# Optimization experiments

Measured on AMD Instinct MI355X. Metric: run time of the kernel, lower is better.

The kernel has to match this reference:

```python
import jax, jax.numpy as jnp
import numpy as np


def _scan(x):
    # x: [B, C, D0, D1, D2] -> [B, 4, C, L] with L = D0*D1*D2
    B, C = x.shape[0], x.shape[1]
    x0 = x.reshape(B, C, -1)                          # row-major flatten of (D0,D1,D2)
    x1 = jnp.swapaxes(x, -2, -1).reshape(B, C, -1)    # swap last two spatial axes then flatten
    x2 = jnp.flip(x0, axis=-1)
    x3 = jnp.flip(x1, axis=-1)
    return jnp.stack([x0, x1, x2, x3], axis=1)        # [B, 4, C, L]


def setup_inputs() -> dict:
    key = jax.random.key(0)
    x = jax.random.normal(key, (2, 96, 32, 32, 32), dtype=jnp.float32)
    return {"x": x}


def reference(x) -> jnp.ndarray:
    # x: [B, C, I, J, K]
    xs_i = _scan(x)                                   # scan over (i, j, k)
    xs_j = _scan(jnp.transpose(x, (0, 1, 3, 4, 2)))   # b c i j k -> b c j k i
    xs_k = _scan(jnp.transpose(x, (0, 1, 4, 2, 3)))   # b c i j k -> b c k i j
    return jnp.concatenate([xs_i, xs_j, xs_k], axis=1)  # [B, 12, C, I*J*K]
```

## Files before the change

### kernel.cpp

```cpp
#include <hip/hip_runtime.h>

#define L 32768
#define NC 96
#define LDS_FLOATS (32 * 1057)
#define LDS_BYTES  (LDS_FLOATS * 4)

typedef float f4 __attribute__((ext_vector_type(4)));


__global__ __launch_bounds__(1024) void cross_scan3d(const float* __restrict__ in,
                                                     float* __restrict__ out) {
    extern __shared__ float lds[];

    const int bc  = blockIdx.x;
    const int b   = bc / NC;
    const int c   = bc % NC;
    const int tid = threadIdx.x;

    const f4* src4 = (const f4*)(in + (size_t)bc * L);
    #define OPTR(s) ((f4*)(out + ((size_t)((b)*12 + (s)) * NC + (c)) * L))
    #define NT(p, v) __builtin_nontemporal_store((v), (p))
    #define A(i, j, k) ((i) * 1057 + (j) * 33 + (k))

    f4* o0 = OPTR(0);  f4* o0f = OPTR(2);
    f4* o1 = OPTR(1);  f4* o1f = OPTR(3);
    f4* o2 = OPTR(4);  f4* o2f = OPTR(6);
    f4* o3 = OPTR(5);  f4* o3f = OPTR(7);
    f4* o4 = OPTR(8);  f4* o4f = OPTR(10);
    f4* o5 = OPTR(9);  f4* o5f = OPTR(11);

    #pragma unroll
    for (int it = 0; it < 8; ++it) {
        int t = it * 1024 + tid;
        f4 v = src4[t];
        int i = t >> 8, j = (t >> 3) & 31, k4 = t & 7;
        float* d = &lds[A(i, j, k4 * 4)];
        d[0] = v.x; d[1] = v.y; d[2] = v.z; d[3] = v.w;
        NT(o0 + t, v);
        f4 vr = { v.w, v.z, v.y, v.x };
        NT(o0f + (8191 - t), vr);
    }
    __syncthreads();

    #pragma unroll
    for (int it = 0; it < 8; ++it) {
        int t = it * 1024 + tid;
        int i = t >> 8, k = (t >> 3) & 31, j4 = t & 7;
        f4 v;
        v.x = lds[A(i, j4 * 4 + 0, k)];
        v.y = lds[A(i, j4 * 4 + 1, k)];
        v.z = lds[A(i, j4 * 4 + 2, k)];
        v.w = lds[A(i, j4 * 4 + 3, k)];
        NT(o1 + t, v);
        f4 vr = { v.w, v.z, v.y, v.x };
        NT(o1f + (8191 - t), vr);
    }

    #pragma unroll
    for (int it = 0; it < 8; ++it) {
        int t = it * 1024 + tid;
        int j = t >> 8, i = (t >> 3) & 31, k4 = t & 7;
        f4 v;
        v.x = lds[A(i, j, k4 * 4 + 0)];
        v.y = lds[A(i, j, k4 * 4 + 1)];
        v.z = lds[A(i, j, k4 * 4 + 2)];
        v.w = lds[A(i, j, k4 * 4 + 3)];
        NT(o3 + t, v);
        f4 vr = { v.w, v.z, v.y, v.x };
        NT(o3f + (8191 - t), vr);
    }

    #pragma unroll
    for (int it = 0; it < 8; ++it) {
        int t = it * 1024 + tid;
        int j = t >> 8, k = (t >> 3) & 31, i4 = t & 7;
        f4 v;
        v.x = lds[A(i4 * 4 + 0, j, k)];
        v.y = lds[A(i4 * 4 + 1, j, k)];
        v.z = lds[A(i4 * 4 + 2, j, k)];
        v.w = lds[A(i4 * 4 + 3, j, k)];
        NT(o2 + t, v);
        f4 vr = { v.w, v.z, v.y, v.x };
        NT(o2f + (8191 - t), vr);
    }

    #pragma unroll
    for (int it = 0; it < 8; ++it) {
        int t = it * 1024 + tid;
        int k = t >> 8, i = (t >> 3) & 31, j4 = t & 7;
        f4 v;
        v.x = lds[A(i, j4 * 4 + 0, k)];
        v.y = lds[A(i, j4 * 4 + 1, k)];
        v.z = lds[A(i, j4 * 4 + 2, k)];
        v.w = lds[A(i, j4 * 4 + 3, k)];
        NT(o4 + t, v);
        f4 vr = { v.w, v.z, v.y, v.x };
        NT(o4f + (8191 - t), vr);
    }

    #pragma unroll
    for (int it = 0; it < 8; ++it) {
        int t = it * 1024 + tid;
        int k = t >> 8, j = (t >> 3) & 31, i4 = t & 7;
        f4 v;
        v.x = lds[A(i4 * 4 + 0, j, k)];
        v.y = lds[A(i4 * 4 + 1, j, k)];
        v.z = lds[A(i4 * 4 + 2, j, k)];
        v.w = lds[A(i4 * 4 + 3, j, k)];
        NT(o5 + t, v);
        f4 vr = { v.w, v.z, v.y, v.x };
        NT(o5f + (8191 - t), vr);
    }

    #undef OPTR
    #undef NT
    #undef A
}

extern "C" void kernel_launch(void* const* d_in, const int* in_sizes, int n_in,
                              void* d_out, int out_size, void* d_ws, size_t ws_size,
                              hipStream_t stream) {
    const float* in = (const float*)d_in[0];
    float* out = (float*)d_out;
    const int bc_count = in_sizes[0] / L;

    (void)hipFuncSetAttribute((const void*)cross_scan3d,
                              hipFuncAttributeMaxDynamicSharedMemorySize, LDS_BYTES);

    cross_scan3d<<<dim3(bc_count), 1024, LDS_BYTES, stream>>>(in, out);
}
```

Measured before the change: 61.73 us.

## Write each output stream sequentially per phase, re-gathering flipped outputs from LDS

New measurement: 60.52 us (median of 2 runs). About the same (-2.0%).

```diff
diff --git a/kernel.cpp b/kernel.cpp
--- a/kernel.cpp
+++ b/kernel.cpp
@@ -22,95 +22,70 @@
     #define NT(p, v) __builtin_nontemporal_store((v), (p))
     #define A(i, j, k) ((i) * 1057 + (j) * 33 + (k))
 
-    f4* o0 = OPTR(0);  f4* o0f = OPTR(2);
-    f4* o1 = OPTR(1);  f4* o1f = OPTR(3);
-    f4* o2 = OPTR(4);  f4* o2f = OPTR(6);
-    f4* o3 = OPTR(5);  f4* o3f = OPTR(7);
-    f4* o4 = OPTR(8);  f4* o4f = OPTR(10);
-    f4* o5 = OPTR(9);  f4* o5f = OPTR(11);
+    #define G0(v, u) { int i=(u)>>8, j=((u)>>3)&31, kb=((u)&7)*4;               \
+        v.x=lds[A(i,j,kb+0)]; v.y=lds[A(i,j,kb+1)];                             \
+        v.z=lds[A(i,j,kb+2)]; v.w=lds[A(i,j,kb+3)]; }
+    #define G1(v, u) { int i=(u)>>8, k=((u)>>3)&31, jb=((u)&7)*4;               \
+        v.x=lds[A(i,jb+0,k)]; v.y=lds[A(i,jb+1,k)];                             \
+        v.z=lds[A(i,jb+2,k)]; v.w=lds[A(i,jb+3,k)]; }
+    #define G2(v, u) { int j=(u)>>8, k=((u)>>3)&31, ib=((u)&7)*4;               \
+        v.x=lds[A(ib+0,j,k)]; v.y=lds[A(ib+1,j,k)];                             \
+        v.z=lds[A(ib+2,j,k)]; v.w=lds[A(ib+3,j,k)]; }
+    #define G3(v, u) { int j=(u)>>8, i=((u)>>3)&31, kb=((u)&7)*4;               \
+        v.x=lds[A(i,j,kb+0)]; v.y=lds[A(i,j,kb+1)];                             \
+        v.z=lds[A(i,j,kb+2)]; v.w=lds[A(i,j,kb+3)]; }
+    #define G4(v, u) { int k=(u)>>8, i=((u)>>3)&31, jb=((u)&7)*4;               \
+        v.x=lds[A(i,jb+0,k)]; v.y=lds[A(i,jb+1,k)];                             \
+        v.z=lds[A(i,jb+2,k)]; v.w=lds[A(i,jb+3,k)]; }
+    #define G5(v, u) { int k=(u)>>8, j=((u)>>3)&31, ib=((u)&7)*4;               \
+        v.x=lds[A(ib+0,j,k)]; v.y=lds[A(ib+1,j,k)];                             \
+        v.z=lds[A(ib+2,j,k)]; v.w=lds[A(ib+3,j,k)]; }
 
-    #pragma unroll
-    for (int it = 0; it < 8; ++it) {
-        int t = it * 1024 + tid;
-        f4 v = src4[t];
-        int i = t >> 8, j = (t >> 3) & 31, k4 = t & 7;
-        float* d = &lds[A(i, j, k4 * 4)];
-        d[0] = v.x; d[1] = v.y; d[2] = v.z; d[3] = v.w;
-        NT(o0 + t, v);
-        f4 vr = { v.w, v.z, v.y, v.x };
-        NT(o0f + (8191 - t), vr);
-    }
-    __syncthreads();
+    #define PHASE_BASE(Gm, optr)                                                \
+        _Pragma("unroll")                                                       \
+        for (int it = 0; it < 8; ++it) {                                        \
+            int t = it * 1024 + tid;                                            \
+            f4 v; Gm(v, t);                                                     \
+            NT((optr) + t, v);                                                  \
+        }                                                                       \
+        __syncthreads();
 
-    #pragma unroll
-    for (int it = 0; it < 8; ++it) {
-        int t = it * 1024 + tid;
-        int i = t >> 8, k = (t >> 3) & 31, j4 = t & 7;
-        f4 v;
-        v.x = lds[A(i, j4 * 4 + 0, k)];
-        v.y = lds[A(i, j4 * 4 + 1, k)];
-        v.z = lds[A(i, j4 * 4 + 2, k)];
-        v.w = lds[A(i, j4 * 4 + 3, k)];
-        NT(o1 + t, v);
-        f4 vr = { v.w, v.z, v.y, v.x };
-        NT(o1f + (8191 - t), vr);
+    #define PHASE_FLIP(Gm, optr)                                                \
+        _Pragma("unroll")                                                       \
+        for (int it = 0; it < 8; ++it) {                                        \
+            int t = it * 1024 + tid;                                            \
+            int u = 8191 - t;                                                   \
+            f4 v; Gm(v, u);                                                     \
+            f4 r = { v.w, v.z, v.y, v.x };                                      \
+            NT((optr) + t, r);                                                  \
+        }                                                                       \
+        __syncthreads();
+
+    {
+        f4* o0 = OPTR(0);
+        #pragma unroll
+        for (int it = 0; it < 8; ++it) {
+            int t = it * 1024 + tid;
+            f4 v = __builtin_nontemporal_load(src4 + t);
+            int i = t >> 8, j = (t >> 3) & 31, kb = (t & 7) * 4;
+            float* d = &lds[A(i, j, kb)];
+            d[0] = v.x; d[1] = v.y; d[2] = v.z; d[3] = v.w;
+            NT(o0 + t, v);
+        }
+        __syncthreads();
     }
 
-    #pragma unroll
-    for (int it = 0; it < 8; ++it) {
-        int t = it * 1024 + tid;
-        int j = t >> 8, i = (t >> 3) & 31, k4 = t & 7;
-        f4 v;
-        v.x = lds[A(i, j, k4 * 4 + 0)];
-        v.y = lds[A(i, j, k4 * 4 + 1)];
-        v.z = lds[A(i, j, k4 * 4 + 2)];
-        v.w = lds[A(i, j, k4 * 4 + 3)];
-        NT(o3 + t, v);
-        f4 vr = { v.w, v.z, v.y, v.x };
-        NT(o3f + (8191 - t), vr);
-    }
-
-    #pragma unroll
-    for (int it = 0; it < 8; ++it) {
-        int t = it * 1024 + tid;
-        int j = t >> 8, k = (t >> 3) & 31, i4 = t & 7;
-        f4 v;
-        v.x = lds[A(i4 * 4 + 0, j, k)];
-        v.y = lds[A(i4 * 4 + 1, j, k)];
-        v.z = lds[A(i4 * 4 + 2, j, k)];
-        v.w = lds[A(i4 * 4 + 3, j, k)];
-        NT(o2 + t, v);
-        f4 vr = { v.w, v.z, v.y, v.x };
-        NT(o2f + (8191 - t), vr);
-    }
-
-    #pragma unroll
-    for (int it = 0; it < 8; ++it) {
-        int t = it * 1024 + tid;
-        int k = t >> 8, i = (t >> 3) & 31, j4 = t & 7;
-        f4 v;
-        v.x = lds[A(i, j4 * 4 + 0, k)];
-        v.y = lds[A(i, j4 * 4 + 1, k)];
-        v.z = lds[A(i, j4 * 4 + 2, k)];
-        v.w = lds[A(i, j4 * 4 + 3, k)];
-        NT(o4 + t, v);
-        f4 vr = { v.w, v.z, v.y, v.x };
-        NT(o4f + (8191 - t), vr);
-    }
-
-    #pragma unroll
-    for (int it = 0; it < 8; ++it) {
-        int t = it * 1024 + tid;
-        int k = t >> 8, j = (t >> 3) & 31, i4 = t & 7;
-        f4 v;
-        v.x = lds[A(i4 * 4 + 0, j, k)];
-        v.y = lds[A(i4 * 4 + 1, j, k)];
-        v.z = lds[A(i4 * 4 + 2, j, k)];
-        v.w = lds[A(i4 * 4 + 3, j, k)];
-        NT(o5 + t, v);
-        f4 vr = { v.w, v.z, v.y, v.x };
-        NT(o5f + (8191 - t), vr);
-    }
+    PHASE_FLIP(G0, OPTR(2))
+    PHASE_BASE(G1, OPTR(1))
+    PHASE_FLIP(G1, OPTR(3))
+    PHASE_BASE(G3, OPTR(5))
+    PHASE_FLIP(G3, OPTR(7))
+    PHASE_BASE(G2, OPTR(4))
+    PHASE_FLIP(G2, OPTR(6))
+    PHASE_BASE(G4, OPTR(8))
+    PHASE_FLIP(G4, OPTR(10))
+    PHASE_BASE(G5, OPTR(9))
+    PHASE_FLIP(G5, OPTR(11))
 
     #undef OPTR
     #undef NT
```
